# Kernel tuning notes

Hardware: AMD Instinct MI355X
Metric: run time of the kernel (lower is better)

Reference implementation:

```python
import jax, jax.numpy as jnp
import numpy as np

HEADS = 8
DIM_HEAD = 64
DIM = 512
LN_EPS = 1e-5


def rotate_half(t):
    shp = t.shape
    t = t.reshape(*shp[:-1], -1, 2)
    t1, t2 = t[..., 0], t[..., 1]
    return jnp.stack((-t2, t1), axis=-1).reshape(shp)


def apply_rope(freqs, t):
    # freqs: (b,1,n,dh) broadcast against t: (b,h,n,dh); rot_dim == dh so no pass-through
    return t * jnp.cos(freqs) + rotate_half(t) * jnp.sin(freqs)


def layer_norm(x, g, b, eps=LN_EPS):
    mu = jnp.mean(x, axis=-1, keepdims=True)
    var = jnp.var(x, axis=-1, keepdims=True)
    return (x - mu) * jax.lax.rsqrt(var + eps) * g + b


def setup_inputs() -> dict:
    key = jax.random.key(0)
    ks = jax.random.split(key, 8)
    n, b = 2048, 4
    inner = HEADS * DIM_HEAD
    inp = {
        "x": jax.random.normal(ks[0], (n, b, DIM), dtype=jnp.float32),
        "rot_pos_emb": jax.random.uniform(ks[1], (b, n, DIM_HEAD), dtype=jnp.float32),
        "Wq": jax.random.normal(ks[2], (inner, DIM), dtype=jnp.float32) * (DIM ** -0.5),
        "Wk": jax.random.normal(ks[3], (inner, DIM), dtype=jnp.float32) * (DIM ** -0.5),
        "Wv": jax.random.normal(ks[4], (inner, DIM), dtype=jnp.float32) * (DIM ** -0.5),
        "Wo": jax.random.normal(ks[5], (DIM, inner), dtype=jnp.float32) * (inner ** -0.5),
        "bo": jnp.zeros((DIM,), dtype=jnp.float32),
        "ln_g": jnp.ones((DIM,), dtype=jnp.float32),
        "ln_b": jnp.zeros((DIM,), dtype=jnp.float32),
        "head_scale": jnp.ones((1, HEADS, 1, 1), dtype=jnp.float32),
        "ls_scale": jnp.full((1, 1, DIM), 1e-5, dtype=jnp.float32),
    }
    return inp


def reference(x, rot_pos_emb, Wq, Wk, Wv, Wo, bo, ln_g, ln_b, head_scale, ls_scale):
    n, b, d = x.shape
    h, dh = HEADS, DIM_HEAD
    scale = dh ** -0.5

    xb = jnp.transpose(x, (1, 0, 2))  # (b,n,d)
    q = (xb @ Wq.T).reshape(b, n, h, dh).transpose(0, 2, 1, 3)  # (b,h,n,dh)
    k = (xb @ Wk.T).reshape(b, n, h, dh).transpose(0, 2, 1, 3)
    v = (xb @ Wv.T).reshape(b, n, h, dh).transpose(0, 2, 1, 3)

    freqs = rot_pos_emb[:, None]  # (b,1,n,dh)
    q = apply_rope(freqs, q)
    k = apply_rope(freqs, k)

    sim = jnp.einsum("bhid,bhjd->bhij", q, k) * scale
    mask = jnp.triu(jnp.ones((n, n), dtype=bool), 1)
    sim = jnp.where(mask[None, None], -jnp.finfo(sim.dtype).max, sim)
    attn = jax.nn.softmax(sim, axis=-1)

    out = jnp.einsum("bhij,bhjd->bhid", attn, v) * head_scale
    out = out.transpose(0, 2, 1, 3).reshape(b, n, h * dh)
    out = layer_norm(out @ Wo.T + bo, ln_g, ln_b)
    out = jnp.transpose(out, (1, 0, 2))  # (n,b,d)
    return ls_scale * out
```

## Files before the change

kernel.cpp:

```cpp
#include <hip/hip_runtime.h>
#include <hip/hip_bf16.h>
#include <math.h>

#define NSEQ 2048
#define NB 4
#define NH 8
#define DH 64
#define DMODEL 512
#define MROWS (NSEQ * 4)

typedef short bf16x8 __attribute__((ext_vector_type(8)));
typedef float f32x4 __attribute__((ext_vector_type(4)));

static __device__ __forceinline__ short f2bf_r(float f) {
    unsigned u = __float_as_uint(f);
    u += 0x7FFF + ((u >> 16) & 1);
    return (short)(u >> 16);
}
static __device__ __forceinline__ unsigned bfpack(float a, float b) {
    unsigned ua = __float_as_uint(a); ua += 0x7FFF + ((ua >> 16) & 1);
    unsigned ub = __float_as_uint(b); ub += 0x7FFF + ((ub >> 16) & 1);
    return (ua >> 16) | (ub & 0xFFFF0000u);
}

__global__ __launch_bounds__(256) void k0_convert(
    const float* __restrict__ x, const float* __restrict__ Wq,
    const float* __restrict__ Wk, const float* __restrict__ Wv,
    const float* __restrict__ Wo, const float* __restrict__ rope,
    __hip_bfloat16* __restrict__ xb, __hip_bfloat16* __restrict__ Wb,
    float* __restrict__ cs, float* __restrict__ sn)
{
    const int idx = blockIdx.x * 256 + threadIdx.x;
    if (idx < 8192 * 128) {
        const int row = idx >> 7, c = (idx & 127) << 2;
        const int bi = row >> 11, ni = row & 2047;
        float4 v = *(const float4*)(x + ((size_t)(ni * NB + bi)) * DMODEL + c);
        uint2 u; u.x = bfpack(v.x, v.y); u.y = bfpack(v.z, v.w);
        *(uint2*)((short*)xb + (size_t)row * 512 + c) = u;
    } else if (idx < 8192 * 128 + 2048 * 128) {
        const int j = idx - 8192 * 128;
        const int row = j >> 7, c = (j & 127) << 2;
        const float* src = (row < 512) ? Wq : (row < 1024) ? Wk
                         : (row < 1536) ? Wv : Wo;
        const int rr = row & 511;
        float4 v = *(const float4*)(src + (size_t)rr * 512 + c);
        uint2 u; u.x = bfpack(v.x, v.y); u.y = bfpack(v.z, v.w);
        *(uint2*)((short*)Wb + (size_t)row * 512 + c) = u;
    } else {
        const int j = idx - (8192 * 128 + 2048 * 128);
        float4 f = *(const float4*)(rope + (size_t)j * 4);
        float4 c4, s4;
        __sincosf(f.x, &s4.x, &c4.x);
        __sincosf(f.y, &s4.y, &c4.y);
        __sincosf(f.z, &s4.z, &c4.z);
        __sincosf(f.w, &s4.w, &c4.w);
        *(float4*)(cs + (size_t)j * 4) = c4;
        *(float4*)(sn + (size_t)j * 4) = s4;
    }
}

__global__ __launch_bounds__(256) void k1_qk(
    const __hip_bfloat16* __restrict__ xb, const float* __restrict__ cs,
    const float* __restrict__ sn, const __hip_bfloat16* __restrict__ Wb,
    __hip_bfloat16* __restrict__ Qs, __hip_bfloat16* __restrict__ Ks)
{
    __shared__ short As[128 * 72];
    __shared__ short Bs[128 * 72];
    const int t = threadIdx.x;
    const int w = t >> 6, L = t & 63, lo = L & 15, g = L >> 4;
    const int mhW = (w >> 1) << 6;
    const int nhX = (w & 1) << 6;

    const int lid = (int)(blockIdx.y * gridDim.x + blockIdx.x);
    const int xcd = lid & 7, slot = lid >> 3;
    const int row_blk = xcd * 8 + (slot & 7);
    const int col_blk = slot >> 3;
    const int row0 = row_blk * 128, col0 = col_blk * 128;
    const int bi = row0 >> 11, ni0 = row0 & 2047;

    f32x4 acc[4][4] = {};
    for (int k0 = 0; k0 < DMODEL; k0 += 64) {
        __syncthreads();
#pragma unroll
        for (int c = 0; c < 4; ++c) {
            const int idx = c * 256 + t;
            const int m = idx >> 3, kb = idx & 7;
            *(uint4*)&As[m * 72 + kb * 8] =
                *(const uint4*)((const short*)xb + (size_t)(row0 + m) * 512 + k0 + kb * 8);
            *(uint4*)&Bs[m * 72 + kb * 8] =
                *(const uint4*)((const short*)Wb + (size_t)(col0 + m) * 512 + k0 + kb * 8);
        }
        __syncthreads();
#pragma unroll
        for (int ks = 0; ks < 2; ++ks) {
            bf16x8 af[4], bfr[4];
#pragma unroll
            for (int mi = 0; mi < 4; ++mi)
                af[mi] = *(const bf16x8*)&Bs[(mhW + mi * 16 + lo) * 72 + ks * 32 + g * 8];
#pragma unroll
            for (int ni = 0; ni < 4; ++ni)
                bfr[ni] = *(const bf16x8*)&As[(nhX + ni * 16 + lo) * 72 + ks * 32 + g * 8];
#pragma unroll
            for (int mi = 0; mi < 4; ++mi)
#pragma unroll
                for (int ni = 0; ni < 4; ++ni)
                    acc[mi][ni] = __builtin_amdgcn_mfma_f32_16x16x32_bf16(
                        af[mi], bfr[ni], acc[mi][ni], 0, 0, 0);
        }
    }

    const float SC = 0.125f * 1.44269504088896f;
    short* outp = (short*)((col0 < 512) ? Qs : Ks);
    const float qs = (col0 < 512) ? SC : 1.0f;
    const int cbase = col0 & 511;
#pragma unroll
    for (int mi = 0; mi < 4; ++mi) {
        const int c0 = cbase + mhW + mi * 16 + (g << 2);
        const int h = c0 >> 6, e0 = c0 & 63;
        short* hb = outp + ((size_t)(bi * NH + h)) * 131072
                    + (e0 >> 5) * 512 + ((e0 >> 3) & 3) * 128 + (e0 & 7);
#pragma unroll
        for (int ni = 0; ni < 4; ++ni) {
            const int nseq = ni0 + nhX + ni * 16 + lo;
            const float4 c4 = *(const float4*)(cs + ((size_t)bi * NSEQ + nseq) * DH + e0);
            const float4 s4 = *(const float4*)(sn + ((size_t)bi * NSEQ + nseq) * DH + e0);
            const f32x4 v = acc[mi][ni];
            const float o0 = (v[0] * c4.x - v[1] * s4.x) * qs;
            const float o1 = (v[1] * c4.y + v[0] * s4.y) * qs;
            const float o2 = (v[2] * c4.z - v[3] * s4.z) * qs;
            const float o3 = (v[3] * c4.w + v[2] * s4.w) * qs;
            uint2 u; u.x = bfpack(o0, o1); u.y = bfpack(o2, o3);
            *(uint2*)(hb + (size_t)(nseq >> 4) * 1024 + (nseq & 15) * 8) = u;
        }
    }
}

__global__ __launch_bounds__(256) void k1_v(
    const __hip_bfloat16* __restrict__ xb, const __hip_bfloat16* __restrict__ Wb,
    __hip_bfloat16* __restrict__ Vs)
{
    __shared__ short As[128 * 72];
    __shared__ short Bs[128 * 72];
    const int t = threadIdx.x;
    const int w = t >> 6, L = t & 63, lo = L & 15, g = L >> 4;
    const int mh = (w >> 1) << 6, nh = (w & 1) << 6;

    const int lid = (int)(blockIdx.y * gridDim.x + blockIdx.x);
    const int xcd = lid & 7, slot = lid >> 3;
    const int row_blk = xcd * 8 + (slot & 7);
    const int col_blk = slot >> 3;
    const int row0 = row_blk * 128, col0 = col_blk * 128;
    const int bi = row0 >> 11, ni0 = row0 & 2047;

    f32x4 acc[4][4] = {};
    for (int k0 = 0; k0 < DMODEL; k0 += 64) {
        __syncthreads();
#pragma unroll
        for (int c = 0; c < 4; ++c) {
            const int idx = c * 256 + t;
            const int m = idx >> 3, kb = idx & 7;
            *(uint4*)&As[m * 72 + kb * 8] =
                *(const uint4*)((const short*)xb + (size_t)(row0 + m) * 512 + k0 + kb * 8);
            *(uint4*)&Bs[m * 72 + kb * 8] =
                *(const uint4*)((const short*)Wb + (size_t)(1024 + col0 + m) * 512 + k0 + kb * 8);
        }
        __syncthreads();
#pragma unroll
        for (int ks = 0; ks < 2; ++ks) {
            bf16x8 af[4], bfr[4];
#pragma unroll
            for (int mi = 0; mi < 4; ++mi)
                af[mi] = *(const bf16x8*)&As[(mh + mi * 16 + lo) * 72 + ks * 32 + g * 8];
#pragma unroll
            for (int ni = 0; ni < 4; ++ni)
                bfr[ni] = *(const bf16x8*)&Bs[(nh + ni * 16 + lo) * 72 + ks * 32 + g * 8];
#pragma unroll
            for (int mi = 0; mi < 4; ++mi)
#pragma unroll
                for (int ni = 0; ni < 4; ++ni)
                    acc[mi][ni] = __builtin_amdgcn_mfma_f32_16x16x32_bf16(
                        af[mi], bfr[ni], acc[mi][ni], 0, 0, 0);
        }
    }
#pragma unroll
    for (int ni = 0; ni < 4; ++ni) {
        const int c = col0 + nh + ni * 16 + lo;
        const int h = c >> 6, e = c & 63;
        short* hb = (short*)Vs + ((size_t)(bi * NH + h)) * 131072
                    + (e >> 4) * 512 + (e & 15) * 8;
#pragma unroll
        for (int mi = 0; mi < 4; ++mi) {
            const int nb = ni0 + mh + mi * 16 + g * 4;
            uint2 u;
            u.x = bfpack(acc[mi][ni][0], acc[mi][ni][1]);
            u.y = bfpack(acc[mi][ni][2], acc[mi][ni][3]);
            *(uint2*)(hb + (size_t)(nb >> 5) * 2048 + ((nb >> 3) & 3) * 128
                      + (nb & 7)) = u;
        }
    }
}

__global__ __launch_bounds__(256, 3) void k2_attn(
    const __hip_bfloat16* __restrict__ Qs, const __hip_bfloat16* __restrict__ Ks,
    const __hip_bfloat16* __restrict__ Vs, const float* __restrict__ head_scale,
    __hip_bfloat16* __restrict__ Ob)
{
    __shared__ short sP[4][16 * 72];

    const int t = threadIdx.x;
    const int w = t >> 6, L = t & 63, lo = L & 15, g = L >> 4;

    const int lid = (int)blockIdx.x;
    const int xcd = lid & 7, slot = lid >> 3;
    const int bh = xcd * 4 + (slot & 3);
    const int qb = 31 - (slot >> 2);
    const int qt = qb * 4 + w;
    const int bi = bh >> 3, h = bh & 7;

    const short* Kp = (const short*)Ks + (size_t)bh * (128 * 1024) + L * 8;
    const short* Vp = (const short*)Vs + (size_t)bh * (256 * 512) + L * 8;
    const short* Qp = (const short*)Qs + (size_t)bh * (128 * 1024)
                      + (size_t)qt * 1024 + L * 8;
    const bf16x8 qf0 = *(const bf16x8*)(Qp);
    const bf16x8 qf1 = *(const bf16x8*)(Qp + 512);

    f32x4 acc[4] = {};
    float l_i = 0.f;
    const int nkt = qb + 1;

    auto body = [&](const bf16x8* kc0, const bf16x8* kc1, int kt) {
        const bool diag = (kt == qb);
        const int mlim = diag ? w : 3;
        const bool hi = (mlim >= 2);

        bf16x8 vb0[4], vb1[4];
        const short* vp0 = Vp + (size_t)(kt * 8) * 512;
#pragma unroll
        for (int dt = 0; dt < 4; ++dt) {
            vb0[dt] = *(const bf16x8*)(vp0 + dt * 512);
            if (hi) vb1[dt] = *(const bf16x8*)(vp0 + (4 + dt) * 512);
        }

        f32x4 s[4];
#pragma unroll
        for (int mt = 0; mt < 4; ++mt) {
            if (mt <= mlim) {
                f32x4 z = {};
                z = __builtin_amdgcn_mfma_f32_16x16x32_bf16(kc0[mt], qf0, z, 0, 0, 0);
                s[mt] = __builtin_amdgcn_mfma_f32_16x16x32_bf16(kc1[mt], qf1, z, 0, 0, 0);
                if (diag && mt == mlim) {
#pragma unroll
                    for (int r = 0; r < 4; ++r)
                        if ((g * 4 + r) > lo) s[mt][r] = -1e30f;
                }
            }
        }

#pragma unroll
        for (int mt = 0; mt < 4; ++mt) {
            uint2 u;
            if (mt <= mlim) {
                const float p0 = exp2f(s[mt][0] - 16.f);
                const float p1 = exp2f(s[mt][1] - 16.f);
                const float p2 = exp2f(s[mt][2] - 16.f);
                const float p3 = exp2f(s[mt][3] - 16.f);
                l_i += (p0 + p1) + (p2 + p3);
                u.x = bfpack(p0, p1); u.y = bfpack(p2, p3);
            } else {
                u.x = 0u; u.y = 0u;
            }
            *(uint2*)&sP[w][lo * 72 + mt * 16 + g * 4] = u;
        }

        const bf16x8 pb0 = *(const bf16x8*)&sP[w][lo * 72 + g * 8];
        if (hi) {
            const bf16x8 pb1 = *(const bf16x8*)&sP[w][lo * 72 + 32 + g * 8];
#pragma unroll
            for (int dt = 0; dt < 4; ++dt) {
                acc[dt] = __builtin_amdgcn_mfma_f32_16x16x32_bf16(vb0[dt], pb0, acc[dt], 0, 0, 0);
                acc[dt] = __builtin_amdgcn_mfma_f32_16x16x32_bf16(vb1[dt], pb1, acc[dt], 0, 0, 0);
            }
        } else {
#pragma unroll
            for (int dt = 0; dt < 4; ++dt)
                acc[dt] = __builtin_amdgcn_mfma_f32_16x16x32_bf16(vb0[dt], pb0, acc[dt], 0, 0, 0);
        }
    };

    bf16x8 kA0[4], kA1[4], kB0[4], kB1[4];
#pragma unroll
    for (int mt = 0; mt < 4; ++mt) {
        const short* kp = Kp + (size_t)mt * 1024;
        kA0[mt] = *(const bf16x8*)kp;
        kA1[mt] = *(const bf16x8*)(kp + 512);
    }
    int kt = 0;
#pragma unroll 1
    while (true) {
        if (kt + 1 < nkt) {
            const short* kp = Kp + (size_t)((kt + 1) * 4) * 1024;
#pragma unroll
            for (int mt = 0; mt < 4; ++mt) {
                kB0[mt] = *(const bf16x8*)(kp + mt * 1024);
                kB1[mt] = *(const bf16x8*)(kp + mt * 1024 + 512);
            }
        }
        body(kA0, kA1, kt);
        ++kt;
        if (kt >= nkt) break;
        if (kt + 1 < nkt) {
            const short* kp = Kp + (size_t)((kt + 1) * 4) * 1024;
#pragma unroll
            for (int mt = 0; mt < 4; ++mt) {
                kA0[mt] = *(const bf16x8*)(kp + mt * 1024);
                kA1[mt] = *(const bf16x8*)(kp + mt * 1024 + 512);
            }
        }
        body(kB0, kB1, kt);
        ++kt;
        if (kt >= nkt) break;
    }

    l_i += __shfl_xor(l_i, 16);
    l_i += __shfl_xor(l_i, 32);
    const float f = head_scale[h] / l_i;
    const int q = qt * 16 + lo;
    short* op = (short*)Ob + ((size_t)bi * NSEQ + q) * DMODEL + h * DH + g * 4;
#pragma unroll
    for (int dt = 0; dt < 4; ++dt) {
        uint2 u;
        u.x = bfpack(acc[dt][0] * f, acc[dt][1] * f);
        u.y = bfpack(acc[dt][2] * f, acc[dt][3] * f);
        *(uint2*)(op + dt * 16) = u;
    }
}

__global__ __launch_bounds__(256) void k3_proj(
    const __hip_bfloat16* __restrict__ Ob, const __hip_bfloat16* __restrict__ Wob,
    const float* __restrict__ bo, float* __restrict__ C2)
{
    __shared__ short As[128 * 72];
    __shared__ short Bs[128 * 72];
    const int t = threadIdx.x;
    const int w = t >> 6, L = t & 63, lo = L & 15, g = L >> 4;
    const int mh = (w >> 1) << 6, nh = (w & 1) << 6;

    const int lid = (int)(blockIdx.y * gridDim.x + blockIdx.x);
    const int xcd = lid & 7, slot = lid >> 3;
    const int row_blk = xcd * 8 + (slot & 7);
    const int col_blk = slot >> 3;
    const int row0 = row_blk * 128, col0 = col_blk * 128;

    f32x4 acc[4][4] = {};
    for (int k0 = 0; k0 < DMODEL; k0 += 64) {
        __syncthreads();
#pragma unroll
        for (int c = 0; c < 4; ++c) {
            const int idx = c * 256 + t;
            const int m = idx >> 3, kb = idx & 7;
            *(uint4*)&As[m * 72 + kb * 8] =
                *(const uint4*)((const short*)Ob + (size_t)(row0 + m) * 512 + k0 + kb * 8);
            *(uint4*)&Bs[m * 72 + kb * 8] =
                *(const uint4*)((const short*)Wob + (size_t)(col0 + m) * 512 + k0 + kb * 8);
        }
        __syncthreads();
#pragma unroll
        for (int ks = 0; ks < 2; ++ks) {
            bf16x8 af[4], bfr[4];
#pragma unroll
            for (int mi = 0; mi < 4; ++mi)
                af[mi] = *(const bf16x8*)&As[(mh + mi * 16 + lo) * 72 + ks * 32 + g * 8];
#pragma unroll
            for (int ni = 0; ni < 4; ++ni)
                bfr[ni] = *(const bf16x8*)&Bs[(nh + ni * 16 + lo) * 72 + ks * 32 + g * 8];
#pragma unroll
            for (int mi = 0; mi < 4; ++mi)
#pragma unroll
                for (int ni = 0; ni < 4; ++ni)
                    acc[mi][ni] = __builtin_amdgcn_mfma_f32_16x16x32_bf16(
                        af[mi], bfr[ni], acc[mi][ni], 0, 0, 0);
        }
    }
#pragma unroll
    for (int ni = 0; ni < 4; ++ni) {
        const int c = col0 + nh + ni * 16 + lo;
        const float b = bo[c];
#pragma unroll
        for (int mi = 0; mi < 4; ++mi) {
#pragma unroll
            for (int r = 0; r < 4; ++r) {
                const int m = row0 + mh + mi * 16 + g * 4 + r;
                C2[(size_t)m * DMODEL + c] = acc[mi][ni][r] + b;
            }
        }
    }
}

__global__ __launch_bounds__(256) void k4_ln(
    const float* __restrict__ C2, const float* __restrict__ g,
    const float* __restrict__ bln, const float* __restrict__ ls,
    float* __restrict__ out)
{
    const int m = blockIdx.x;
    const int bi = m >> 11, ni = m & (NSEQ - 1);
    const float* row = C2 + (size_t)m * DMODEL;
    const int t = threadIdx.x;
    float v0 = row[t], v1 = row[t + 256];
    float s = v0 + v1, sq2 = v0 * v0 + v1 * v1;
#pragma unroll
    for (int off = 32; off > 0; off >>= 1) {
        s += __shfl_down(s, off);
        sq2 += __shfl_down(sq2, off);
    }
    __shared__ float red[8];
    const int wid = t >> 6;
    if ((t & 63) == 0) { red[wid] = s; red[wid + 4] = sq2; }
    __syncthreads();
    s = red[0] + red[1] + red[2] + red[3];
    sq2 = red[4] + red[5] + red[6] + red[7];
    const float mean = s * (1.f / 512.f);
    const float var = sq2 * (1.f / 512.f) - mean * mean;
    const float rstd = rsqrtf(var + 1e-5f);
    float* ob = out + ((size_t)ni * NB + bi) * DMODEL;
    ob[t]       = ((v0 - mean) * rstd * g[t]       + bln[t])       * ls[t];
    ob[t + 256] = ((v1 - mean) * rstd * g[t + 256] + bln[t + 256]) * ls[t + 256];
}

extern "C" void kernel_launch(void* const* d_in, const int* in_sizes, int n_in,
                              void* d_out, int out_size, void* d_ws, size_t ws_size,
                              hipStream_t stream) {
    const float* x          = (const float*)d_in[0];
    const float* rope       = (const float*)d_in[1];
    const float* Wq         = (const float*)d_in[2];
    const float* Wk         = (const float*)d_in[3];
    const float* Wv         = (const float*)d_in[4];
    const float* Wo         = (const float*)d_in[5];
    const float* bo         = (const float*)d_in[6];
    const float* ln_g       = (const float*)d_in[7];
    const float* ln_b       = (const float*)d_in[8];
    const float* head_scale = (const float*)d_in[9];
    const float* ls_scale   = (const float*)d_in[10];
    float* out = (float*)d_out;

    char* wsb = (char*)d_ws;
    __hip_bfloat16* xb  = (__hip_bfloat16*)(wsb);
    __hip_bfloat16* Wb  = (__hip_bfloat16*)(wsb + ((size_t) 8 << 20));
    __hip_bfloat16* Qs  = (__hip_bfloat16*)(wsb + ((size_t)10 << 20));
    __hip_bfloat16* Ks  = (__hip_bfloat16*)(wsb + ((size_t)18 << 20));
    __hip_bfloat16* Vs  = (__hip_bfloat16*)(wsb + ((size_t)26 << 20));
    __hip_bfloat16* Ob  = (__hip_bfloat16*)(wsb + ((size_t)34 << 20));
    float*          cs  = (float*)(wsb + ((size_t)42 << 20));
    float*          sn  = (float*)(wsb + ((size_t)44 << 20));
    float*          C2  = (float*)(wsb + ((size_t)10 << 20));
    __hip_bfloat16* Wob = Wb + (size_t)1536 * 512;

    k0_convert<<<5632, 256, 0, stream>>>(x, Wq, Wk, Wv, Wo, rope, xb, Wb, cs, sn);
    k1_qk<<<dim3(64, 8), 256, 0, stream>>>(xb, cs, sn, Wb, Qs, Ks);
    k1_v<<<dim3(64, 4), 256, 0, stream>>>(xb, Wb, Vs);
    k2_attn<<<1024, 256, 0, stream>>>(Qs, Ks, Vs, head_scale, Ob);
    k3_proj<<<dim3(64, 4), 256, 0, stream>>>(Ob, Wob, bo, C2);
    k4_ln<<<MROWS, 256, 0, stream>>>(C2, ln_g, ln_b, ls_scale, out);
}
```

Before: 194.2 us.

## Merge QK and V projection kernels, store pre-LN output in bf16

Fuses the separate QK and V projection GEMMs into one launch with 12 column blocks, where V blocks swap the A/B operand roles to keep their transposed output layout. The attention kernel drops the fixed -16 exponent offset, uses a cheaper non-ties-to-even bf16 pack for probabilities, and switches K/V addressing to incrementing pointers. The output projection now writes bf16 instead of fp32, halving traffic into the layernorm kernel. The bf16 intermediate and the removed exp offset both reduce precision margin, and without the offset exp2f can overflow when scores are large.

```diff
diff --git a/kernel.cpp b/kernel.cpp
--- a/kernel.cpp
+++ b/kernel.cpp
@@ -21,6 +21,14 @@
     unsigned ua = __float_as_uint(a); ua += 0x7FFF + ((ua >> 16) & 1);
     unsigned ub = __float_as_uint(b); ub += 0x7FFF + ((ub >> 16) & 1);
     return (ua >> 16) | (ub & 0xFFFF0000u);
+}
+static __device__ __forceinline__ unsigned bfpack_f(float a, float b) {
+    unsigned ua = (__float_as_uint(a) + 0x8000u) >> 16;
+    unsigned ub = (__float_as_uint(b) + 0x8000u) & 0xFFFF0000u;
+    return ua | ub;
+}
+static __device__ __forceinline__ float bf2f(unsigned short u) {
+    return __uint_as_float(((unsigned)u) << 16);
 }
 
 __global__ __launch_bounds__(256) void k0_convert(
@@ -59,24 +67,26 @@
     }
 }
 
-__global__ __launch_bounds__(256) void k1_qk(
+__global__ __launch_bounds__(256) void k1_qkv(
     const __hip_bfloat16* __restrict__ xb, const float* __restrict__ cs,
     const float* __restrict__ sn, const __hip_bfloat16* __restrict__ Wb,
-    __hip_bfloat16* __restrict__ Qs, __hip_bfloat16* __restrict__ Ks)
+    __hip_bfloat16* __restrict__ Qs, __hip_bfloat16* __restrict__ Ks,
+    __hip_bfloat16* __restrict__ Vs)
 {
     __shared__ short As[128 * 72];
     __shared__ short Bs[128 * 72];
     const int t = threadIdx.x;
     const int w = t >> 6, L = t & 63, lo = L & 15, g = L >> 4;
-    const int mhW = (w >> 1) << 6;
-    const int nhX = (w & 1) << 6;
+    const int ah = (w >> 1) << 6;
+    const int bhh = (w & 1) << 6;
 
     const int lid = (int)(blockIdx.y * gridDim.x + blockIdx.x);
     const int xcd = lid & 7, slot = lid >> 3;
     const int row_blk = xcd * 8 + (slot & 7);
     const int col_blk = slot >> 3;
-    const int row0 = row_blk * 128, col0 = col_blk * 128;
+    const int row0 = row_blk * 128, wrow0 = col_blk * 128;
     const int bi = row0 >> 11, ni0 = row0 & 2047;
+    const bool isV = (col_blk >= 8);
 
     f32x4 acc[4][4] = {};
     for (int k0 = 0; k0 < DMODEL; k0 += 64) {
@@ -88,18 +98,20 @@
             *(uint4*)&As[m * 72 + kb * 8] =
                 *(const uint4*)((const short*)xb + (size_t)(row0 + m) * 512 + k0 + kb * 8);
             *(uint4*)&Bs[m * 72 + kb * 8] =
-                *(const uint4*)((const short*)Wb + (size_t)(col0 + m) * 512 + k0 + kb * 8);
+                *(const uint4*)((const short*)Wb + (size_t)(wrow0 + m) * 512 + k0 + kb * 8);
         }
         __syncthreads();
+        const short* Abuf = isV ? As : Bs;
+        const short* Bbuf = isV ? Bs : As;
 #pragma unroll
         for (int ks = 0; ks < 2; ++ks) {
             bf16x8 af[4], bfr[4];
 #pragma unroll
             for (int mi = 0; mi < 4; ++mi)
-                af[mi] = *(const bf16x8*)&Bs[(mhW + mi * 16 + lo) * 72 + ks * 32 + g * 8];
+                af[mi] = *(const bf16x8*)&Abuf[(ah + mi * 16 + lo) * 72 + ks * 32 + g * 8];
 #pragma unroll
             for (int ni = 0; ni < 4; ++ni)
-                bfr[ni] = *(const bf16x8*)&As[(nhX + ni * 16 + lo) * 72 + ks * 32 + g * 8];
+                bfr[ni] = *(const bf16x8*)&Bbuf[(bhh + ni * 16 + lo) * 72 + ks * 32 + g * 8];
 #pragma unroll
             for (int mi = 0; mi < 4; ++mi)
 #pragma unroll
@@ -109,93 +121,48 @@
         }
     }
 
-    const float SC = 0.125f * 1.44269504088896f;
-    short* outp = (short*)((col0 < 512) ? Qs : Ks);
-    const float qs = (col0 < 512) ? SC : 1.0f;
-    const int cbase = col0 & 511;
-#pragma unroll
-    for (int mi = 0; mi < 4; ++mi) {
-        const int c0 = cbase + mhW + mi * 16 + (g << 2);
-        const int h = c0 >> 6, e0 = c0 & 63;
-        short* hb = outp + ((size_t)(bi * NH + h)) * 131072
-                    + (e0 >> 5) * 512 + ((e0 >> 3) & 3) * 128 + (e0 & 7);
+    if (!isV) {
+        const float SC = 0.125f * 1.44269504088896f;
+        short* outp = (short*)((wrow0 < 512) ? Qs : Ks);
+        const float qs = (wrow0 < 512) ? SC : 1.0f;
+        const int cbase = wrow0 & 511;
+#pragma unroll
+        for (int mi = 0; mi < 4; ++mi) {
+            const int c0 = cbase + ah + mi * 16 + (g << 2);
+            const int h = c0 >> 6, e0 = c0 & 63;
+            short* hb = outp + ((size_t)(bi * NH + h)) * 131072
+                        + (e0 >> 5) * 512 + ((e0 >> 3) & 3) * 128 + (e0 & 7);
+#pragma unroll
+            for (int ni = 0; ni < 4; ++ni) {
+                const int nseq = ni0 + bhh + ni * 16 + lo;
+                const float4 c4 = *(const float4*)(cs + ((size_t)bi * NSEQ + nseq) * DH + e0);
+                const float4 s4 = *(const float4*)(sn + ((size_t)bi * NSEQ + nseq) * DH + e0);
+                const f32x4 v = acc[mi][ni];
+                const float o0 = (v[0] * c4.x - v[1] * s4.x) * qs;
+                const float o1 = (v[1] * c4.y + v[0] * s4.y) * qs;
+                const float o2 = (v[2] * c4.z - v[3] * s4.z) * qs;
+                const float o3 = (v[3] * c4.w + v[2] * s4.w) * qs;
+                uint2 u; u.x = bfpack(o0, o1); u.y = bfpack(o2, o3);
+                *(uint2*)(hb + (size_t)(nseq >> 4) * 1024 + (nseq & 15) * 8) = u;
+            }
+        }
+    } else {
+        const int col0 = wrow0 - 1024;
 #pragma unroll
         for (int ni = 0; ni < 4; ++ni) {
-            const int nseq = ni0 + nhX + ni * 16 + lo;
-            const float4 c4 = *(const float4*)(cs + ((size_t)bi * NSEQ + nseq) * DH + e0);
-            const float4 s4 = *(const float4*)(sn + ((size_t)bi * NSEQ + nseq) * DH + e0);
-            const f32x4 v = acc[mi][ni];
-            const float o0 = (v[0] * c4.x - v[1] * s4.x) * qs;
-            const float o1 = (v[1] * c4.y + v[0] * s4.y) * qs;
-            const float o2 = (v[2] * c4.z - v[3] * s4.z) * qs;
-            const float o3 = (v[3] * c4.w + v[2] * s4.w) * qs;
-            uint2 u; u.x = bfpack(o0, o1); u.y = bfpack(o2, o3);
-            *(uint2*)(hb + (size_t)(nseq >> 4) * 1024 + (nseq & 15) * 8) = u;
-        }
-    }
-}
-
-__global__ __launch_bounds__(256) void k1_v(
-    const __hip_bfloat16* __restrict__ xb, const __hip_bfloat16* __restrict__ Wb,
-    __hip_bfloat16* __restrict__ Vs)
-{
-    __shared__ short As[128 * 72];
-    __shared__ short Bs[128 * 72];
-    const int t = threadIdx.x;
-    const int w = t >> 6, L = t & 63, lo = L & 15, g = L >> 4;
-    const int mh = (w >> 1) << 6, nh = (w & 1) << 6;
-
-    const int lid = (int)(blockIdx.y * gridDim.x + blockIdx.x);
-    const int xcd = lid & 7, slot = lid >> 3;
-    const int row_blk = xcd * 8 + (slot & 7);
-    const int col_blk = slot >> 3;
-    const int row0 = row_blk * 128, col0 = col_blk * 128;
-    const int bi = row0 >> 11, ni0 = row0 & 2047;
-
-    f32x4 acc[4][4] = {};
-    for (int k0 = 0; k0 < DMODEL; k0 += 64) {
-        __syncthreads();
-#pragma unroll
-        for (int c = 0; c < 4; ++c) {
-            const int idx = c * 256 + t;
-            const int m = idx >> 3, kb = idx & 7;
-            *(uint4*)&As[m * 72 + kb * 8] =
-                *(const uint4*)((const short*)xb + (size_t)(row0 + m) * 512 + k0 + kb * 8);
-            *(uint4*)&Bs[m * 72 + kb * 8] =
-                *(const uint4*)((const short*)Wb + (size_t)(1024 + col0 + m) * 512 + k0 + kb * 8);
-        }
-        __syncthreads();
-#pragma unroll
-        for (int ks = 0; ks < 2; ++ks) {
-            bf16x8 af[4], bfr[4];
-#pragma unroll
-            for (int mi = 0; mi < 4; ++mi)
-                af[mi] = *(const bf16x8*)&As[(mh + mi * 16 + lo) * 72 + ks * 32 + g * 8];
-#pragma unroll
-            for (int ni = 0; ni < 4; ++ni)
-                bfr[ni] = *(const bf16x8*)&Bs[(nh + ni * 16 + lo) * 72 + ks * 32 + g * 8];
-#pragma unroll
-            for (int mi = 0; mi < 4; ++mi)
-#pragma unroll
-                for (int ni = 0; ni < 4; ++ni)
-                    acc[mi][ni] = __builtin_amdgcn_mfma_f32_16x16x32_bf16(
-                        af[mi], bfr[ni], acc[mi][ni], 0, 0, 0);
-        }
-    }
-#pragma unroll
-    for (int ni = 0; ni < 4; ++ni) {
-        const int c = col0 + nh + ni * 16 + lo;
-        const int h = c >> 6, e = c & 63;
-        short* hb = (short*)Vs + ((size_t)(bi * NH + h)) * 131072
-                    + (e >> 4) * 512 + (e & 15) * 8;
-#pragma unroll
-        for (int mi = 0; mi < 4; ++mi) {
-            const int nb = ni0 + mh + mi * 16 + g * 4;
-            uint2 u;
-            u.x = bfpack(acc[mi][ni][0], acc[mi][ni][1]);
-            u.y = bfpack(acc[mi][ni][2], acc[mi][ni][3]);
-            *(uint2*)(hb + (size_t)(nb >> 5) * 2048 + ((nb >> 3) & 3) * 128
-                      + (nb & 7)) = u;
+            const int c = col0 + bhh + ni * 16 + lo;
+            const int h = c >> 6, e = c & 63;
+            short* hb = (short*)Vs + ((size_t)(bi * NH + h)) * 131072
+                        + (e >> 4) * 512 + (e & 15) * 8;
+#pragma unroll
+            for (int mi = 0; mi < 4; ++mi) {
+                const int nb = ni0 + ah + mi * 16 + g * 4;
+                uint2 u;
+                u.x = bfpack(acc[mi][ni][0], acc[mi][ni][1]);
+                u.y = bfpack(acc[mi][ni][2], acc[mi][ni][3]);
+                *(uint2*)(hb + (size_t)(nb >> 5) * 2048 + ((nb >> 3) & 3) * 128
+                          + (nb & 7)) = u;
+            }
         }
     }
 }
@@ -217,9 +184,8 @@
     const int qt = qb * 4 + w;
     const int bi = bh >> 3, h = bh & 7;
 
-    const short* Kp = (const short*)Ks + (size_t)bh * (128 * 1024) + L * 8;
-    const short* Vp = (const short*)Vs + (size_t)bh * (256 * 512) + L * 8;
-    const short* Qp = (const short*)Qs + (size_t)bh * (128 * 1024)
+    const short* Kp = (const short*)Ks + (size_t)bh * 131072 + L * 8;
+    const short* Qp = (const short*)Qs + (size_t)bh * 131072
                       + (size_t)qt * 1024 + L * 8;
     const bf16x8 qf0 = *(const bf16x8*)(Qp);
     const bf16x8 qf1 = *(const bf16x8*)(Qp + 512);
@@ -228,13 +194,12 @@
     float l_i = 0.f;
     const int nkt = qb + 1;
 
-    auto body = [&](const bf16x8* kc0, const bf16x8* kc1, int kt) {
+    auto body = [&](const bf16x8* kc0, const bf16x8* kc1, const short* vp0, int kt) {
         const bool diag = (kt == qb);
         const int mlim = diag ? w : 3;
         const bool hi = (mlim >= 2);
 
         bf16x8 vb0[4], vb1[4];
-        const short* vp0 = Vp + (size_t)(kt * 8) * 512;
 #pragma unroll
         for (int dt = 0; dt < 4; ++dt) {
             vb0[dt] = *(const bf16x8*)(vp0 + dt * 512);
@@ -260,12 +225,12 @@
         for (int mt = 0; mt < 4; ++mt) {
             uint2 u;
             if (mt <= mlim) {
-                const float p0 = exp2f(s[mt][0] - 16.f);
-                const float p1 = exp2f(s[mt][1] - 16.f);
-                const float p2 = exp2f(s[mt][2] - 16.f);
-                const float p3 = exp2f(s[mt][3] - 16.f);
+                const float p0 = exp2f(s[mt][0]);
+                const float p1 = exp2f(s[mt][1]);
+                const float p2 = exp2f(s[mt][2]);
+                const float p3 = exp2f(s[mt][3]);
                 l_i += (p0 + p1) + (p2 + p3);
-                u.x = bfpack(p0, p1); u.y = bfpack(p2, p3);
+                u.x = bfpack_f(p0, p1); u.y = bfpack_f(p2, p3);
             } else {
                 u.x = 0u; u.y = 0u;
             }
@@ -288,35 +253,39 @@
     };
 
     bf16x8 kA0[4], kA1[4], kB0[4], kB1[4];
+    const short* vp = (const short*)Vs + (size_t)bh * 131072 + L * 8;
+    const short* kld = Kp;
 #pragma unroll
     for (int mt = 0; mt < 4; ++mt) {
-        const short* kp = Kp + (size_t)mt * 1024;
-        kA0[mt] = *(const bf16x8*)kp;
-        kA1[mt] = *(const bf16x8*)(kp + 512);
-    }
+        kA0[mt] = *(const bf16x8*)(kld + mt * 1024);
+        kA1[mt] = *(const bf16x8*)(kld + mt * 1024 + 512);
+    }
+    kld += 4096;
     int kt = 0;
 #pragma unroll 1
     while (true) {
         if (kt + 1 < nkt) {
-            const short* kp = Kp + (size_t)((kt + 1) * 4) * 1024;
 #pragma unroll
             for (int mt = 0; mt < 4; ++mt) {
-                kB0[mt] = *(const bf16x8*)(kp + mt * 1024);
-                kB1[mt] = *(const bf16x8*)(kp + mt * 1024 + 512);
-            }
-        }
-        body(kA0, kA1, kt);
+                kB0[mt] = *(const bf16x8*)(kld + mt * 1024);
+                kB1[mt] = *(const bf16x8*)(kld + mt * 1024 + 512);
+            }
+            kld += 4096;
+        }
+        body(kA0, kA1, vp, kt);
+        vp += 4096;
         ++kt;
         if (kt >= nkt) break;
         if (kt + 1 < nkt) {
-            const short* kp = Kp + (size_t)((kt + 1) * 4) * 1024;
 #pragma unroll
             for (int mt = 0; mt < 4; ++mt) {
-                kA0[mt] = *(const bf16x8*)(kp + mt * 1024);
-                kA1[mt] = *(const bf16x8*)(kp + mt * 1024 + 512);
-            }
-        }
-        body(kB0, kB1, kt);
+                kA0[mt] = *(const bf16x8*)(kld + mt * 1024);
+                kA1[mt] = *(const bf16x8*)(kld + mt * 1024 + 512);
+            }
+            kld += 4096;
+        }
+        body(kB0, kB1, vp, kt);
+        vp += 4096;
         ++kt;
         if (kt >= nkt) break;
     }
@@ -337,7 +306,7 @@
 
 __global__ __launch_bounds__(256) void k3_proj(
     const __hip_bfloat16* __restrict__ Ob, const __hip_bfloat16* __restrict__ Wob,
-    const float* __restrict__ bo, float* __restrict__ C2)
+    const float* __restrict__ bo, __hip_bfloat16* __restrict__ C2)
 {
     __shared__ short As[128 * 72];
     __shared__ short Bs[128 * 72];
@@ -390,22 +359,22 @@
 #pragma unroll
             for (int r = 0; r < 4; ++r) {
                 const int m = row0 + mh + mi * 16 + g * 4 + r;
-                C2[(size_t)m * DMODEL + c] = acc[mi][ni][r] + b;
+                *((short*)C2 + (size_t)m * DMODEL + c) = f2bf_r(acc[mi][ni][r] + b);
             }
         }
     }
 }
 
 __global__ __launch_bounds__(256) void k4_ln(
-    const float* __restrict__ C2, const float* __restrict__ g,
+    const __hip_bfloat16* __restrict__ C2, const float* __restrict__ g,
     const float* __restrict__ bln, const float* __restrict__ ls,
     float* __restrict__ out)
 {
     const int m = blockIdx.x;
     const int bi = m >> 11, ni = m & (NSEQ - 1);
-    const float* row = C2 + (size_t)m * DMODEL;
+    const unsigned short* row = (const unsigned short*)C2 + (size_t)m * DMODEL;
     const int t = threadIdx.x;
-    float v0 = row[t], v1 = row[t + 256];
+    float v0 = bf2f(row[t]), v1 = bf2f(row[t + 256]);
     float s = v0 + v1, sq2 = v0 * v0 + v1 * v1;
 #pragma unroll
     for (int off = 32; off > 0; off >>= 1) {
@@ -451,12 +420,11 @@
     __hip_bfloat16* Ob  = (__hip_bfloat16*)(wsb + ((size_t)34 << 20));
     float*          cs  = (float*)(wsb + ((size_t)42 << 20));
     float*          sn  = (float*)(wsb + ((size_t)44 << 20));
-    float*          C2  = (float*)(wsb + ((size_t)10 << 20));
+    __hip_bfloat16* C2  = (__hip_bfloat16*)(wsb + ((size_t)10 << 20));
     __hip_bfloat16* Wob = Wb + (size_t)1536 * 512;
 
     k0_convert<<<5632, 256, 0, stream>>>(x, Wq, Wk, Wv, Wo, rope, xb, Wb, cs, sn);
-    k1_qk<<<dim3(64, 8), 256, 0, stream>>>(xb, cs, sn, Wb, Qs, Ks);
-    k1_v<<<dim3(64, 4), 256, 0, stream>>>(xb, Wb, Vs);
+    k1_qkv<<<dim3(64, 12), 256, 0, stream>>>(xb, cs, sn, Wb, Qs, Ks, Vs);
     k2_attn<<<1024, 256, 0, stream>>>(Qs, Ks, Vs, head_scale, Ob);
     k3_proj<<<dim3(64, 4), 256, 0, stream>>>(Ob, Wob, bo, C2);
     k4_ln<<<MROWS, 256, 0, stream>>>(C2, ln_g, ln_b, ls_scale, out);
```

Result: faster. 184.8 us (-4.8%).
